# Kernel tuning notes

Measured on AMD Instinct MI355X. Metric: run time of the kernel, lower is better.

## Reference

```python
import jax, jax.numpy as jnp
import numpy as np

D_MODEL = 1024
N_HEAD = 16


def setup_inputs() -> dict:
    key = jax.random.key(0)
    ks = jax.random.split(key, 11)
    B, T, D = 4, 2048, D_MODEL
    s = 1.0 / np.sqrt(D)
    inp = {
        "q": jax.random.normal(ks[0], (B, T, D), jnp.float32),
        "k": jax.random.normal(ks[1], (B, T, D), jnp.float32),
        "v": jax.random.normal(ks[2], (B, T, D), jnp.float32),
        "wq": jax.random.normal(ks[3], (D, D), jnp.float32) * s,
        "bq": jnp.zeros((D,), jnp.float32),
        "wk": jax.random.normal(ks[4], (D, D), jnp.float32) * s,
        "bk": jnp.zeros((D,), jnp.float32),
        "wv": jax.random.normal(ks[5], (D, D), jnp.float32) * s,
        "bv": jnp.zeros((D,), jnp.float32),
        "wo": jax.random.normal(ks[6], (D, D), jnp.float32) * s,
        "bo": jnp.zeros((D,), jnp.float32),
    }
    return inp


def reference(q, k, v, wq, bq, wk, bk, wv, bv, wo, bo):
    B, T, D = q.shape
    H = N_HEAD
    hd = D // H  # head dim
    # torch nn.Linear: y = x @ W.T + b
    qh = (q @ wq.T + bq).reshape(B, T, H, hd).transpose(0, 2, 1, 3)  # [B,H,T,hd]
    kh = (k @ wk.T + bk).reshape(B, T, H, hd).transpose(0, 2, 1, 3)
    vh = (v @ wv.T + bv).reshape(B, T, H, hd).transpose(0, 2, 1, 3)
    scale = 1.0 / jnp.sqrt(jnp.asarray(hd, qh.dtype))
    score = jnp.einsum("bhqd,bhkd->bhqk", qh, kh) * scale  # [B,H,T,T]
    causal = jnp.tril(jnp.ones((T, T), dtype=bool))
    score = jnp.where(causal, score, jnp.asarray(-jnp.inf, score.dtype))
    attn = jax.nn.softmax(score, axis=-1)
    out = jnp.einsum("bhqk,bhkd->bhqd", attn, vh)  # [B,H,T,hd]
    out = out.transpose(0, 2, 1, 3).reshape(B, T, D)
    return out @ wo.T + bo
```

## Files before the change

### kernel.cpp

```cpp
#include <hip/hip_runtime.h>
#include <hip/hip_bf16.h>

#define D_MODEL 1024
#define N_HEAD  16
#define HD      64
#define T_SEQ   2048
#define B_SZ    4
#define M_ROWS  (B_SZ * T_SEQ)

typedef __bf16 bf16;
typedef __bf16 bf16x4 __attribute__((ext_vector_type(4)));
typedef __bf16 bf16x8 __attribute__((ext_vector_type(8)));
typedef float  floatx4 __attribute__((ext_vector_type(4)));

__device__ __forceinline__ floatx4 fzero4() {
    floatx4 z = {0.f, 0.f, 0.f, 0.f};
    return z;
}

__device__ __forceinline__ bf16x8 cvt8(const float4 a, const float4 b) {
    bf16x8 o;
    o[0] = (bf16)a.x; o[1] = (bf16)a.y; o[2] = (bf16)a.z; o[3] = (bf16)a.w;
    o[4] = (bf16)b.x; o[5] = (bf16)b.y; o[6] = (bf16)b.z; o[7] = (bf16)b.w;
    return o;
}

__device__ __forceinline__ void async_ld16(const void* g, void* l) {
    __builtin_amdgcn_global_load_lds(
        (const __attribute__((address_space(1))) void*)g,
        (__attribute__((address_space(3))) void*)l,
        16, 0, 0);
}

struct CvtArgs {
    const float* s[7];
    bf16* d[7];
    int n[7];
};
__global__ __launch_bounds__(256) void cvt7_kernel(CvtArgs a)
{
    const float* src = a.s[blockIdx.y];
    bf16* dst = a.d[blockIdx.y];
    int n8 = a.n[blockIdx.y];
    int i = blockIdx.x * blockDim.x + threadIdx.x;
    int stride = gridDim.x * blockDim.x;
    for (; i < n8; i += stride) {
        float4 x = ((const float4*)src)[2 * i];
        float4 y = ((const float4*)src)[2 * i + 1];
        ((bf16x8*)dst)[i] = cvt8(x, y);
    }
}

struct GemmArgs {
    const bf16* A[2];
    const bf16* W[2];
    const float* bias[2];
    void*       Out[2];
    float       scl[2];
    int         omode[2];
};

__global__ __launch_bounds__(512, 4) void gemm_k(GemmArgs g)
{
    __shared__ bf16 ldsA[256 * 64];
    __shared__ bf16 ldsW[128 * 64];

    const int z = blockIdx.z;
    const bf16* A     = g.A[z];
    const bf16* W     = g.W[z];
    const float* bias = g.bias[z];
    void* Out         = g.Out[z];
    const float scl   = g.scl[z];
    const int omode   = g.omode[z];

    const int tid  = threadIdx.x;
    const int wave = tid >> 6, lane = tid & 63;
    const int quad = lane >> 4, l15 = lane & 15;
    const int wr = wave >> 1, wc = wave & 1;
    const int m0 = blockIdx.x * 256, n0 = blockIdx.y * 128;

    floatx4 acc[4][4];
#pragma unroll
    for (int i = 0; i < 4; ++i)
#pragma unroll
        for (int j = 0; j < 4; ++j) acc[i][j] = fzero4();

    const int ro = lane >> 3;
    const int c8 = lane & 7;
    const bf16* gA = A + (size_t)(m0 + wave * 32 + ro) * 1024 + (c8 ^ ro) * 8;
    const bf16* gW = W + (size_t)(n0 + wave * 16 + ro) * 1024 + (c8 ^ ro) * 8;

    for (int kt = 0; kt < 16; ++kt) {
        __syncthreads();
#pragma unroll
        for (int j = 0; j < 4; ++j)
            async_ld16((const void*)(gA + kt * 64 + (size_t)j * 8 * 1024),
                       &ldsA[(wave * 32 + j * 8) * 64]);
#pragma unroll
        for (int j = 0; j < 2; ++j)
            async_ld16((const void*)(gW + kt * 64 + (size_t)j * 8 * 1024),
                       &ldsW[(wave * 16 + j * 8) * 64]);
        __syncthreads();

#pragma unroll
        for (int ks = 0; ks < 2; ++ks) {
            const int pos = ((ks * 4 + quad) ^ (l15 & 7)) * 8;
            bf16x8 af[4], bw[4];
#pragma unroll
            for (int i = 0; i < 4; ++i)
                af[i] = *(const bf16x8*)(&ldsA[(wr * 64 + i * 16 + l15) * 64 + pos]);
#pragma unroll
            for (int j = 0; j < 4; ++j)
                bw[j] = *(const bf16x8*)(&ldsW[(wc * 64 + j * 16 + l15) * 64 + pos]);
#pragma unroll
            for (int i = 0; i < 4; ++i)
#pragma unroll
                for (int j = 0; j < 4; ++j)
                    acc[i][j] = __builtin_amdgcn_mfma_f32_16x16x32_bf16(af[i], bw[j], acc[i][j], 0, 0, 0);
        }
    }

#pragma unroll
    for (int i = 0; i < 4; ++i) {
#pragma unroll
        for (int j = 0; j < 4; ++j) {
            if (omode == 1) {
                int m = m0 + wr * 64 + i * 16 + quad * 4;
                int n = n0 + wc * 64 + j * 16 + l15;
                int b = m >> 11, t0 = m & 2047;
                int h = n >> 6,  d = n & 63;
                bf16x4 pv;
#pragma unroll
                for (int r = 0; r < 4; ++r)
                    pv[r] = (bf16)((acc[i][j][r] + bias[n]) * scl);
                size_t addr = ((size_t)(b * N_HEAD + h) * HD + d) * T_SEQ + t0;
                *(bf16x4*)(&((bf16*)Out)[addr]) = pv;
            } else {
#pragma unroll
                for (int r = 0; r < 4; ++r) {
                    int m = m0 + wr * 64 + i * 16 + quad * 4 + r;
                    int n = n0 + wc * 64 + j * 16 + l15;
                    float val = (acc[i][j][r] + bias[n]) * scl;
                    if (omode == 2) {
                        ((float*)Out)[(size_t)m * 1024 + n] = val;
                    } else {
                        int b = m >> 11, t = m & 2047;
                        int h = n >> 6,  d = n & 63;
                        size_t addr = ((size_t)(b * N_HEAD + h) * T_SEQ + t) * HD + d;
                        ((bf16*)Out)[addr] = (bf16)val;
                    }
                }
            }
        }
    }
}

__global__ __launch_bounds__(256, 2) void attn_kernel(
    const bf16* __restrict__ Qh, const bf16* __restrict__ Kh,
    const bf16* __restrict__ Vt, bf16* __restrict__ AO)
{
    __shared__ bf16 Ks[128 * 64];
    __shared__ bf16 Vts[64 * 128];
    __shared__ bf16 Ps[128 * 72];

    const int tid  = threadIdx.x;
    const int wave = tid >> 6, lane = tid & 63;
    const int quad = lane >> 4, l15 = lane & 15;
    const int bh = blockIdx.y;
    const size_t base = (size_t)bh * T_SEQ * HD;
    const int bb = bh >> 4, hh = bh & 15;

    const int kro = lane >> 3;
    const int kgc = (lane & 7) ^ kro;
    const bf16* kgbase = Kh + base + (size_t)(wave * 32 + kro) * HD + kgc * 8;
    const int vrow_lo = lane >> 4;
    const int vchunk  = lane & 15;

    const bf16* vgbase[4];
    bf16* kdst[4];
    bf16* vdst[4];
#pragma unroll
    for (int j = 0; j < 4; ++j) {
        int d = wave * 16 + j * 4 + vrow_lo;
        int gcv = vchunk ^ (d & 15);
        vgbase[j] = Vt + base + (size_t)d * T_SEQ + gcv * 8;
        vdst[j]   = &Vts[d * 128 + vchunk * 8];
        kdst[j]   = &Ks[(wave * 32 + j * 8 + kro) * 64 + (lane & 7) * 8];
    }

    for (int phase = 0; phase < 2; ++phase) {
        const int qt = phase ? blockIdx.x : 15 - blockIdx.x;

        bf16x8 qf[2][2];
        const bf16* qbase = Qh + base + (size_t)(qt * 128 + wave * 32) * HD;
#pragma unroll
        for (int ti = 0; ti < 2; ++ti)
#pragma unroll
            for (int ks = 0; ks < 2; ++ks)
                qf[ti][ks] = *(const bf16x8*)(qbase + (ti * 16 + l15) * HD + ks * 32 + quad * 8);

        bf16x8 kreg[4], vreg[4];
#pragma unroll
        for (int j = 0; j < 4; ++j)
            kreg[j] = *(const bf16x8*)(kgbase + (size_t)(j * 8) * HD);
#pragma unroll
        for (int j = 0; j < 4; ++j)
            vreg[j] = *(const bf16x8*)(vgbase[j]);

        float mrow[2] = {-1e30f, -1e30f}, lrow[2] = {0.f, 0.f};
        floatx4 oacc[2][4];
#pragma unroll
        for (int ti = 0; ti < 2; ++ti)
#pragma unroll
            for (int nj = 0; nj < 4; ++nj) oacc[ti][nj] = fzero4();

        for (int kt = 0; kt <= qt; ++kt) {
            __syncthreads();
#pragma unroll
            for (int j = 0; j < 4; ++j) *(bf16x8*)kdst[j] = kreg[j];
#pragma unroll
            for (int j = 0; j < 4; ++j) *(bf16x8*)vdst[j] = vreg[j];
            __syncthreads();

            if (kt < qt) {
#pragma unroll
                for (int j = 0; j < 4; ++j)
                    kreg[j] = *(const bf16x8*)(kgbase + (size_t)((kt + 1) * 128 + j * 8) * HD);
#pragma unroll
                for (int j = 0; j < 4; ++j)
                    vreg[j] = *(const bf16x8*)(vgbase[j] + (kt + 1) * 128);
            }

            const bool diag = (kt == qt);
            const int lim = diag ? (2 * wave + 1) : 7;

            floatx4 sacc[2][8];
#pragma unroll
            for (int ti = 0; ti < 2; ++ti)
#pragma unroll
                for (int tj = 0; tj < 8; ++tj) sacc[ti][tj] = fzero4();
            __builtin_amdgcn_s_setprio(1);
#pragma unroll
            for (int ks = 0; ks < 2; ++ks) {
                const int pos = ((ks * 4 + quad) ^ (l15 & 7)) * 8;
#pragma unroll
                for (int tj = 0; tj < 8; ++tj) {
                    if (tj <= lim) {
                        bf16x8 kf = *(const bf16x8*)(&Ks[(tj * 16 + l15) * 64 + pos]);
                        sacc[0][tj] = __builtin_amdgcn_mfma_f32_16x16x32_bf16(kf, qf[0][ks], sacc[0][tj], 0, 0, 0);
                        sacc[1][tj] = __builtin_amdgcn_mfma_f32_16x16x32_bf16(kf, qf[1][ks], sacc[1][tj], 0, 0, 0);
                    }
                }
            }
            __builtin_amdgcn_s_setprio(0);

#pragma unroll
            for (int ti = 0; ti < 2; ++ti) {
                const int ql = wave * 32 + ti * 16 + l15;
                float mxp[4] = {-1e30f, -1e30f, -1e30f, -1e30f};
#pragma unroll
                for (int tj = 0; tj < 8; ++tj) {
                    if (tj <= lim) {
#pragma unroll
                        for (int r = 0; r < 4; ++r) {
                            float s = sacc[ti][tj][r];
                            if (diag && (tj * 16 + quad * 4 + r) > ql) s = -1e30f;
                            sacc[ti][tj][r] = s;
                            mxp[r] = fmaxf(mxp[r], s);
                        }
                    }
                }
                float mx = fmaxf(fmaxf(mxp[0], mxp[1]), fmaxf(mxp[2], mxp[3]));
                mx = fmaxf(mx, __shfl_xor(mx, 16));
                mx = fmaxf(mx, __shfl_xor(mx, 32));
                if (__any(mx > mrow[ti] + 8.0f)) {
                    float mnew  = fmaxf(mrow[ti], mx);
                    float alpha = exp2f(mrow[ti] - mnew);
                    mrow[ti] = mnew;
                    lrow[ti] *= alpha;
#pragma unroll
                    for (int r = 0; r < 4; ++r) {
                        float ar = __shfl(alpha, quad * 4 + r);
#pragma unroll
                        for (int nj = 0; nj < 4; ++nj)
                            oacc[ti][nj][r] *= ar;
                    }
                }
                float rs[4] = {0.f, 0.f, 0.f, 0.f};
#pragma unroll
                for (int tj = 0; tj < 8; ++tj) {
                    if (tj <= lim) {
#pragma unroll
                        for (int r = 0; r < 4; ++r) {
                            float p = exp2f(sacc[ti][tj][r] - mrow[ti]);
                            rs[r] += p;
                            sacc[ti][tj][r] = p;
                        }
                    }
                }
                float rsum = (rs[0] + rs[1]) + (rs[2] + rs[3]);
                rsum += __shfl_xor(rsum, 16);
                rsum += __shfl_xor(rsum, 32);
                lrow[ti] += rsum;
            }

#pragma unroll
            for (int h2 = 0; h2 < 2; ++h2) {
                if (4 * h2 > lim) break;
#pragma unroll
                for (int ti = 0; ti < 2; ++ti) {
                    const int ql = wave * 32 + ti * 16 + l15;
#pragma unroll
                    for (int tjo = 0; tjo < 4; ++tjo) {
                        int tj = 4 * h2 + tjo;
                        if (tj <= lim) {
                            bf16x4 pv;
#pragma unroll
                            for (int r = 0; r < 4; ++r) pv[r] = (bf16)sacc[ti][tj][r];
                            *(bf16x4*)(&Ps[ql * 72 + tjo * 16 + quad * 4]) = pv;
                        }
                    }
                }
#pragma unroll
                for (int ks2 = 0; ks2 < 2; ++ks2) {
                    const int gks = 2 * h2 + ks2;
                    if (diag && gks > wave) break;
                    bf16x8 pf[2];
                    pf[0] = *(const bf16x8*)(&Ps[(wave * 32 + l15) * 72 + ks2 * 32 + quad * 8]);
                    pf[1] = *(const bf16x8*)(&Ps[(wave * 32 + 16 + l15) * 72 + ks2 * 32 + quad * 8]);
                    __builtin_amdgcn_s_setprio(1);
#pragma unroll
                    for (int nj = 0; nj < 4; ++nj) {
                        int pos = ((gks * 4 + quad) ^ l15) * 8;
                        bf16x8 vf = *(const bf16x8*)(&Vts[(nj * 16 + l15) * 128 + pos]);
                        oacc[0][nj] = __builtin_amdgcn_mfma_f32_16x16x32_bf16(pf[0], vf, oacc[0][nj], 0, 0, 0);
                        oacc[1][nj] = __builtin_amdgcn_mfma_f32_16x16x32_bf16(pf[1], vf, oacc[1][nj], 0, 0, 0);
                    }
                    __builtin_amdgcn_s_setprio(0);
                }
            }
        }

#pragma unroll
        for (int ti = 0; ti < 2; ++ti) {
#pragma unroll
            for (int r = 0; r < 4; ++r) {
                float lv = __shfl(lrow[ti], quad * 4 + r);
                float rl = 1.f / lv;
                int qrow = qt * 128 + wave * 32 + ti * 16 + quad * 4 + r;
#pragma unroll
                for (int nj = 0; nj < 4; ++nj) {
                    int d = nj * 16 + l15;
                    AO[((size_t)(bb * T_SEQ + qrow)) * D_MODEL + hh * HD + d] =
                        (bf16)(oacc[ti][nj][r] * rl);
                }
            }
        }
    }
}

extern "C" void kernel_launch(void* const* d_in, const int* in_sizes, int n_in,
                              void* d_out, int out_size, void* d_ws, size_t ws_size,
                              hipStream_t stream)
{
    const float* q  = (const float*)d_in[0];
    const float* k  = (const float*)d_in[1];
    const float* v  = (const float*)d_in[2];
    const float* wq = (const float*)d_in[3];
    const float* bq = (const float*)d_in[4];
    const float* wk = (const float*)d_in[5];
    const float* bk = (const float*)d_in[6];
    const float* wv = (const float*)d_in[7];
    const float* bv = (const float*)d_in[8];
    const float* wo = (const float*)d_in[9];
    const float* bo = (const float*)d_in[10];

    char* ws  = (char*)d_ws;
    char* dob = (char*)d_out;
    const size_t MB = 1024 * 1024;

    bf16* Wqb = (bf16*)(ws);
    bf16* Wkb = (bf16*)(ws + 2 * MB);
    bf16* Wvb = (bf16*)(ws + 4 * MB);
    bf16* Wob = (bf16*)(ws + 6 * MB);
    bf16* Vb  = (bf16*)(ws + 8 * MB);
    bf16* AO  = (bf16*)(ws + 8 * MB);
    bf16* Qh  = (bf16*)(ws + 24 * MB);
    bf16* Kh  = (bf16*)(ws + 40 * MB);
    bf16* Qb  = (bf16*)(dob);
    bf16* Kb  = (bf16*)(dob + 16 * MB);
    bf16* Vt  = (bf16*)(dob);

    const int NQ8 = M_ROWS * D_MODEL / 8;
    const int NW8 = D_MODEL * D_MODEL / 8;
    const float QSCALE = 0.18033688011112042f;

    CvtArgs ca;
    ca.s[0] = q;  ca.d[0] = Qb;  ca.n[0] = NQ8;
    ca.s[1] = k;  ca.d[1] = Kb;  ca.n[1] = NQ8;
    ca.s[2] = v;  ca.d[2] = Vb;  ca.n[2] = NQ8;
    ca.s[3] = wq; ca.d[3] = Wqb; ca.n[3] = NW8;
    ca.s[4] = wk; ca.d[4] = Wkb; ca.n[4] = NW8;
    ca.s[5] = wv; ca.d[5] = Wvb; ca.n[5] = NW8;
    ca.s[6] = wo; ca.d[6] = Wob; ca.n[6] = NW8;

    GemmArgs gqk;
    gqk.A[0] = Qb; gqk.W[0] = Wqb; gqk.bias[0] = bq; gqk.Out[0] = (void*)Qh; gqk.scl[0] = QSCALE; gqk.omode[0] = 0;
    gqk.A[1] = Kb; gqk.W[1] = Wkb; gqk.bias[1] = bk; gqk.Out[1] = (void*)Kh; gqk.scl[1] = 1.0f;   gqk.omode[1] = 0;

    GemmArgs gv;
    gv.A[0] = Vb; gv.W[0] = Wvb; gv.bias[0] = bv; gv.Out[0] = (void*)Vt; gv.scl[0] = 1.0f; gv.omode[0] = 1;
    gv.A[1] = Vb; gv.W[1] = Wvb; gv.bias[1] = bv; gv.Out[1] = (void*)Vt; gv.scl[1] = 1.0f; gv.omode[1] = 1;

    GemmArgs go;
    go.A[0] = AO; go.W[0] = Wob; go.bias[0] = bo; go.Out[0] = d_out; go.scl[0] = 1.0f; go.omode[0] = 2;
    go.A[1] = AO; go.W[1] = Wob; go.bias[1] = bo; go.Out[1] = d_out; go.scl[1] = 1.0f; go.omode[1] = 2;

    hipLaunchKernelGGL(cvt7_kernel, dim3(512, 7), dim3(256), 0, stream, ca);
    hipLaunchKernelGGL(gemm_k, dim3(32, 8, 2), dim3(512), 0, stream, gqk);
    hipLaunchKernelGGL(gemm_k, dim3(32, 8, 1), dim3(512), 0, stream, gv);
    hipLaunchKernelGGL(attn_kernel, dim3(8, 64), dim3(256), 0, stream, Qh, Kh, Vt, AO);
    hipLaunchKernelGGL(gemm_k, dim3(32, 8, 1), dim3(512), 0, stream, go);
}
```

Measured before the change: 351.7 us.

## Fuse V fp32-to-bf16 conversion into projection GEMM and merge QKV launches

The V input is no longer converted to bf16 by the separate conversion kernel. The GEMM now loads fp32 V rows into registers, converts them, writes them to LDS, and prefetches the next k-tile before the MFMA loop. The Q, K and V projections now run in a single 3-slice launch, and workspace buffers are remapped to fit. This removes one full fp32 read and bf16 write-read round trip of V plus one kernel launch, at the cost of synchronous register staging instead of async LDS loads for the V slice.

```diff
diff --git a/kernel.cpp b/kernel.cpp
--- a/kernel.cpp
+++ b/kernel.cpp
@@ -33,11 +33,11 @@
 }
 
 struct CvtArgs {
-    const float* s[7];
-    bf16* d[7];
-    int n[7];
+    const float* s[6];
+    bf16* d[6];
+    int n[6];
 };
-__global__ __launch_bounds__(256) void cvt7_kernel(CvtArgs a)
+__global__ __launch_bounds__(256) void cvt6_kernel(CvtArgs a)
 {
     const float* src = a.s[blockIdx.y];
     bf16* dst = a.d[blockIdx.y];
@@ -52,12 +52,13 @@
 }
 
 struct GemmArgs {
-    const bf16* A[2];
-    const bf16* W[2];
-    const float* bias[2];
-    void*       Out[2];
-    float       scl[2];
-    int         omode[2];
+    const void* A[3];
+    const bf16* W[3];
+    const float* bias[3];
+    void*       Out[3];
+    float       scl[3];
+    int         omode[3];
+    int         af32[3];
 };
 
 __global__ __launch_bounds__(512, 4) void gemm_k(GemmArgs g)
@@ -66,12 +67,12 @@
     __shared__ bf16 ldsW[128 * 64];
 
     const int z = blockIdx.z;
-    const bf16* A     = g.A[z];
     const bf16* W     = g.W[z];
     const float* bias = g.bias[z];
     void* Out         = g.Out[z];
     const float scl   = g.scl[z];
     const int omode   = g.omode[z];
+    const int af32    = g.af32[z];
 
     const int tid  = threadIdx.x;
     const int wave = tid >> 6, lane = tid & 63;
@@ -87,20 +88,48 @@
 
     const int ro = lane >> 3;
     const int c8 = lane & 7;
-    const bf16* gA = A + (size_t)(m0 + wave * 32 + ro) * 1024 + (c8 ^ ro) * 8;
+
+    const bf16* gAb = (const bf16*)g.A[z] + (size_t)(m0 + wave * 32 + ro) * 1024 + (c8 ^ ro) * 8;
+    const float* gAf = (const float*)g.A[z] + (size_t)(m0 + wave * 32 + ro) * 1024 + c8 * 8;
+    bf16* dA = &ldsA[(wave * 32 + ro) * 64 + (c8 ^ ro) * 8];
+
     const bf16* gW = W + (size_t)(n0 + wave * 16 + ro) * 1024 + (c8 ^ ro) * 8;
+
+    float4 raf[4][2];
+    if (af32) {
+#pragma unroll
+        for (int j = 0; j < 4; ++j) {
+            raf[j][0] = *(const float4*)(gAf + (size_t)j * 8192);
+            raf[j][1] = *(const float4*)(gAf + (size_t)j * 8192 + 4);
+        }
+    }
 
     for (int kt = 0; kt < 16; ++kt) {
         __syncthreads();
-#pragma unroll
-        for (int j = 0; j < 4; ++j)
-            async_ld16((const void*)(gA + kt * 64 + (size_t)j * 8 * 1024),
-                       &ldsA[(wave * 32 + j * 8) * 64]);
+        if (af32) {
+#pragma unroll
+            for (int j = 0; j < 4; ++j)
+                *(bf16x8*)(dA + j * 8 * 64) = cvt8(raf[j][0], raf[j][1]);
+        } else {
+#pragma unroll
+            for (int j = 0; j < 4; ++j)
+                async_ld16((const void*)(gAb + kt * 64 + (size_t)j * 8 * 1024),
+                           &ldsA[(wave * 32 + j * 8) * 64]);
+        }
 #pragma unroll
         for (int j = 0; j < 2; ++j)
             async_ld16((const void*)(gW + kt * 64 + (size_t)j * 8 * 1024),
                        &ldsW[(wave * 16 + j * 8) * 64]);
         __syncthreads();
+
+        if (af32 && kt < 15) {
+            const int off = (kt + 1) * 64;
+#pragma unroll
+            for (int j = 0; j < 4; ++j) {
+                raf[j][0] = *(const float4*)(gAf + off + (size_t)j * 8192);
+                raf[j][1] = *(const float4*)(gAf + off + (size_t)j * 8192 + 4);
+            }
+        }
 
 #pragma unroll
         for (int ks = 0; ks < 2; ++ks) {
@@ -383,13 +412,12 @@
     bf16* Wkb = (bf16*)(ws + 2 * MB);
     bf16* Wvb = (bf16*)(ws + 4 * MB);
     bf16* Wob = (bf16*)(ws + 6 * MB);
-    bf16* Vb  = (bf16*)(ws + 8 * MB);
+    bf16* Qb  = (bf16*)(ws + 8 * MB);
     bf16* AO  = (bf16*)(ws + 8 * MB);
-    bf16* Qh  = (bf16*)(ws + 24 * MB);
-    bf16* Kh  = (bf16*)(ws + 40 * MB);
-    bf16* Qb  = (bf16*)(dob);
-    bf16* Kb  = (bf16*)(dob + 16 * MB);
-    bf16* Vt  = (bf16*)(dob);
+    bf16* Kb  = (bf16*)(ws + 24 * MB);
+    bf16* Vt  = (bf16*)(ws + 40 * MB);
+    bf16* Qh  = (bf16*)(dob);
+    bf16* Kh  = (bf16*)(dob + 16 * MB);
 
     const int NQ8 = M_ROWS * D_MODEL / 8;
     const int NW8 = D_MODEL * D_MODEL / 8;
@@ -398,27 +426,23 @@
     CvtArgs ca;
     ca.s[0] = q;  ca.d[0] = Qb;  ca.n[0] = NQ8;
     ca.s[1] = k;  ca.d[1] = Kb;  ca.n[1] = NQ8;
-    ca.s[2] = v;  ca.d[2] = Vb;  ca.n[2] = NQ8;
-    ca.s[3] = wq; ca.d[3] = Wqb; ca.n[3] = NW8;
-    ca.s[4] = wk; ca.d[4] = Wkb; ca.n[4] = NW8;
-    ca.s[5] = wv; ca.d[5] = Wvb; ca.n[5] = NW8;
-    ca.s[6] = wo; ca.d[6] = Wob; ca.n[6] = NW8;
-
-    GemmArgs gqk;
-    gqk.A[0] = Qb; gqk.W[0] = Wqb; gqk.bias[0] = bq; gqk.Out[0] = (void*)Qh; gqk.scl[0] = QSCALE; gqk.omode[0] = 0;
-    gqk.A[1] = Kb; gqk.W[1] = Wkb; gqk.bias[1] = bk; gqk.Out[1] = (void*)Kh; gqk.scl[1] = 1.0f;   gqk.omode[1] = 0;
-
-    GemmArgs gv;
-    gv.A[0] = Vb; gv.W[0] = Wvb; gv.bias[0] = bv; gv.Out[0] = (void*)Vt; gv.scl[0] = 1.0f; gv.omode[0] = 1;
-    gv.A[1] = Vb; gv.W[1] = Wvb; gv.bias[1] = bv; gv.Out[1] = (void*)Vt; gv.scl[1] = 1.0f; gv.omode[1] = 1;
+    ca.s[2] = wq; ca.d[2] = Wqb; ca.n[2] = NW8;
+    ca.s[3] = wk; ca.d[3] = Wkb; ca.n[3] = NW8;
+    ca.s[4] = wv; ca.d[4] = Wvb; ca.n[4] = NW8;
+    ca.s[5] = wo; ca.d[5] = Wob; ca.n[5] = NW8;
+
+    GemmArgs gq;
+    gq.A[0] = Qb; gq.W[0] = Wqb; gq.bias[0] = bq; gq.Out[0] = (void*)Qh; gq.scl[0] = QSCALE; gq.omode[0] = 0; gq.af32[0] = 0;
+    gq.A[1] = Kb; gq.W[1] = Wkb; gq.bias[1] = bk; gq.Out[1] = (void*)Kh; gq.scl[1] = 1.0f;   gq.omode[1] = 0; gq.af32[1] = 0;
+    gq.A[2] = v;  gq.W[2] = Wvb; gq.bias[2] = bv; gq.Out[2] = (void*)Vt; gq.scl[2] = 1.0f;   gq.omode[2] = 1; gq.af32[2] = 1;
 
     GemmArgs go;
-    go.A[0] = AO; go.W[0] = Wob; go.bias[0] = bo; go.Out[0] = d_out; go.scl[0] = 1.0f; go.omode[0] = 2;
-    go.A[1] = AO; go.W[1] = Wob; go.bias[1] = bo; go.Out[1] = d_out; go.scl[1] = 1.0f; go.omode[1] = 2;
-
-    hipLaunchKernelGGL(cvt7_kernel, dim3(512, 7), dim3(256), 0, stream, ca);
-    hipLaunchKernelGGL(gemm_k, dim3(32, 8, 2), dim3(512), 0, stream, gqk);
-    hipLaunchKernelGGL(gemm_k, dim3(32, 8, 1), dim3(512), 0, stream, gv);
+    go.A[0] = AO; go.W[0] = Wob; go.bias[0] = bo; go.Out[0] = d_out; go.scl[0] = 1.0f; go.omode[0] = 2; go.af32[0] = 0;
+    go.A[1] = AO; go.W[1] = Wob; go.bias[1] = bo; go.Out[1] = d_out; go.scl[1] = 1.0f; go.omode[1] = 2; go.af32[1] = 0;
+    go.A[2] = AO; go.W[2] = Wob; go.bias[2] = bo; go.Out[2] = d_out; go.scl[2] = 1.0f; go.omode[2] = 2; go.af32[2] = 0;
+
+    hipLaunchKernelGGL(cvt6_kernel, dim3(512, 6), dim3(256), 0, stream, ca);
+    hipLaunchKernelGGL(gemm_k, dim3(32, 8, 3), dim3(512), 0, stream, gq);
     hipLaunchKernelGGL(attn_kernel, dim3(8, 64), dim3(256), 0, stream, Qh, Kh, Vt, AO);
     hipLaunchKernelGGL(gemm_k, dim3(32, 8, 1), dim3(512), 0, stream, go);
 }
```

New measurement: 360.6 us. 2.5% more time.
